# Kernel tuning notes

Hardware: AMD Instinct MI355X
Metric: run time of the kernel (lower is better)

The kernel has to match this reference:

```python
import jax, jax.numpy as jnp
import numpy as np

B, T = 64, 2048
QD, KD, VD, AD = 512, 512, 512, 256


def setup_inputs() -> dict:
    key = jax.random.key(0)
    ks = jax.random.split(key, 9)
    s = lambda d: 1.0 / np.sqrt(d)
    return {
        "query": jax.random.normal(ks[0], (B, QD), jnp.float32),
        "key": jax.random.normal(ks[1], (B, T, KD), jnp.float32),
        "value": jax.random.normal(ks[2], (B, T, VD), jnp.float32),
        "Wq": jax.random.uniform(ks[3], (QD, AD), jnp.float32, -s(QD), s(QD)),
        "bq": jax.random.uniform(ks[4], (AD,), jnp.float32, -s(QD), s(QD)),
        "Wk": jax.random.uniform(ks[5], (KD, AD), jnp.float32, -s(KD), s(KD)),
        "bk": jax.random.uniform(ks[6], (AD,), jnp.float32, -s(KD), s(KD)),
        "Wo": jax.random.uniform(ks[7], (AD, 1), jnp.float32, -s(AD), s(AD)),
        "bo": jax.random.uniform(ks[8], (1,), jnp.float32, -s(AD), s(AD)),
    }


def reference(query, key, value, Wq, bq, Wk, bk, Wo, bo):
    # q_proj: [B, 1, AD]; k_proj: [B, T, AD]
    q_proj = (query @ Wq + bq)[:, None, :]
    k_proj = jnp.einsum("btk,ka->bta", key, Wk) + bk
    # score: [B, T, 1]
    score = jnp.tanh(q_proj + k_proj) @ Wo + bo
    attn = jax.nn.softmax(score, axis=1)  # softmax over keys (dim 1)
    # context: [B, VD] = sum_t attn[b,t] * value[b,t,:]
    context = jnp.einsum("bt,btv->bv", attn[..., 0], value)
    return context, attn[..., 0]
```

## Files before the change

kernel.cpp:

```cpp
#include <hip/hip_runtime.h>

#define NB 64
#define NT 2048
#define NQD 512
#define NKD 512
#define NVD 512
#define NAD 256

typedef __attribute__((ext_vector_type(8))) short s16x8;
typedef __attribute__((ext_vector_type(4))) float fx4;
typedef __attribute__((ext_vector_type(4))) unsigned int u32x4;

__device__ __forceinline__ short f2bf(float x) {
  union { float f; unsigned u; } v; v.f = x;
  return (short)((v.u + 0x7fffu + ((v.u >> 16) & 1u)) >> 16);
}

__device__ __forceinline__ unsigned cvt_pk_bf16(float lo, float hi) {
  unsigned r;
  asm("v_cvt_pk_bf16_f32 %0, %1, %2" : "=v"(r) : "v"(lo), "v"(hi));
  return r;
}

__device__ __forceinline__ float fast_tanh(float x) {
  float e = __expf(x + x);
  return 1.0f - 2.0f * __builtin_amdgcn_rcpf(e + 1.0f);
}

__device__ __forceinline__ void cvt_write32(short* lds, int lbase, int swz, const fx4* q) {
  u32x4 w0, w1;
  w0[0] = cvt_pk_bf16(q[0][0], q[0][1]); w0[1] = cvt_pk_bf16(q[0][2], q[0][3]);
  w0[2] = cvt_pk_bf16(q[1][0], q[1][1]); w0[3] = cvt_pk_bf16(q[1][2], q[1][3]);
  w1[0] = cvt_pk_bf16(q[2][0], q[2][1]); w1[1] = cvt_pk_bf16(q[2][2], q[2][3]);
  w1[2] = cvt_pk_bf16(q[3][0], q[3][1]); w1[3] = cvt_pk_bf16(q[3][2], q[3][3]);
  *(u32x4*)((char*)lds + ((lbase) ^ swz)) = w0;
  *(u32x4*)((char*)lds + ((lbase + 16) ^ swz)) = w1;
}

__global__ void prep_kernel(const float* __restrict__ query, const float* __restrict__ Wq,
                            const float* __restrict__ bq, const float* __restrict__ bk,
                            const float* __restrict__ Wk,
                            float* __restrict__ qpk, short* __restrict__ Bpk) {
  __shared__ float q[NQD];
  const int tid = threadIdx.x;
  if (blockIdx.x < NB) {
    const int b = blockIdx.x;
    for (int k = tid; k < NQD; k += 256) q[k] = query[b * NQD + k];
    __syncthreads();
    float acc = bq[tid] + bk[tid];
#pragma unroll 8
    for (int k = 0; k < NQD; ++k) acc += q[k] * Wq[k * NAD + tid];
    qpk[b * NAD + tid] = acc;
  } else {
    const int ks = blockIdx.x - NB;
#pragma unroll
    for (int rep = 0; rep < 4; ++rep) {
      const int o = rep * 256 + tid;
      const int wnt = o >> 6;
      const int l = o & 63;
      const int g = l >> 4, h = l & 15;
      const int n = wnt * 16 + h;
      const int k0 = ks * 32 + g * 8;
      s16x8 v;
#pragma unroll
      for (int j = 0; j < 8; ++j) v[j] = f2bf(Wk[(size_t)(k0 + j) * NAD + n]);
      *(s16x8*)(Bpk + (size_t)(ks * 1024 + o) * 8) = v;
    }
  }
}

__global__ void __launch_bounds__(256, 3)
score_kernel(const float* __restrict__ key, const short* __restrict__ Bpk,
             const float* __restrict__ qpk, const float* __restrict__ Wo,
             float* __restrict__ score) {
  __shared__ short As[2][64 * 128];
  __shared__ float sred[4][64];
  const int tid = threadIdx.x;
  const int w = tid >> 6, l = tid & 63;
  const int g = l >> 4, h = l & 15;
  const int m0 = blockIdx.x * 64;
  const int b = m0 >> 11;

  const short* bbase = Bpk + (size_t)(w * 4 * 64 + l) * 8;

  s16x8 bcur[4];
#pragma unroll
  for (int nt = 0; nt < 4; ++nt) bcur[nt] = *(const s16x8*)(bbase + nt * 512);

  const int r = tid >> 3, kseg = tid & 7;
  const float* asrc0 = key + (size_t)(m0 + r) * NKD + kseg * 16;
  const float* asrc1 = asrc0 + (size_t)32 * NKD;
  const int lbase0 = r * 256 + kseg * 32;
  const int lbase1 = lbase0 + 32 * 256;
  const int swz = (r & 7) << 4;

  {
    fx4 st[8];
#pragma unroll
    for (int i = 0; i < 4; ++i) st[i] = *(const fx4*)(asrc0 + i * 4);
#pragma unroll
    for (int i = 0; i < 4; ++i) st[4 + i] = *(const fx4*)(asrc1 + i * 4);
    cvt_write32(&As[0][0], lbase0, swz, &st[0]);
    cvt_write32(&As[0][0], lbase1, swz, &st[4]);
  }
  __syncthreads();

  fx4 acc[4][4];
#pragma unroll
  for (int i = 0; i < 4; ++i)
#pragma unroll
    for (int j = 0; j < 4; ++j) acc[i][j] = fx4{0.f, 0.f, 0.f, 0.f};

  const int rsw = (h & 7) << 4;

  int buf = 0;
  for (int c = 0; c < 4; ++c) {
    const bool notLast = (c < 3);
    fx4 st[8];
    if (notLast) {
      const float* gp0 = asrc0 + (c + 1) * 128;
      const float* gp1 = asrc1 + (c + 1) * 128;
#pragma unroll
      for (int i = 0; i < 4; ++i) st[i] = *(const fx4*)(gp0 + i * 4);
#pragma unroll
      for (int i = 0; i < 4; ++i) st[4 + i] = *(const fx4*)(gp1 + i * 4);
    }
#pragma unroll
    for (int kl = 0; kl < 4; ++kl) {
      const int ks = c * 4 + kl;
      s16x8 bnxt[4];
      if (ks < 15) {
#pragma unroll
        for (int nt = 0; nt < 4; ++nt)
          bnxt[nt] = *(const s16x8*)(bbase + (size_t)(ks + 1) * 8192 + nt * 512);
      }
      s16x8 af[4];
#pragma unroll
      for (int mt = 0; mt < 4; ++mt)
        af[mt] = *(const s16x8*)((const char*)&As[buf][0] +
                                 (((mt * 16 + h) * 256 + kl * 64 + g * 16) ^ rsw));
#pragma unroll
      for (int mt = 0; mt < 4; ++mt)
#pragma unroll
        for (int nt = 0; nt < 4; ++nt)
          acc[mt][nt] = __builtin_amdgcn_mfma_f32_16x16x32_bf16(af[mt], bcur[nt], acc[mt][nt], 0, 0, 0);
      if (ks < 15) {
#pragma unroll
        for (int nt = 0; nt < 4; ++nt) bcur[nt] = bnxt[nt];
      }
    }
    if (notLast) {
      cvt_write32(&As[buf ^ 1][0], lbase0, swz, &st[0]);
      cvt_write32(&As[buf ^ 1][0], lbase1, swz, &st[4]);
    }
    __syncthreads();
    buf ^= 1;
  }

  float qv[4], wv[4];
#pragma unroll
  for (int nt = 0; nt < 4; ++nt) {
    const int n = w * 64 + nt * 16 + h;
    qv[nt] = qpk[b * NAD + n];
    wv[nt] = Wo[n];
  }
#pragma unroll
  for (int mt = 0; mt < 4; ++mt) {
#pragma unroll
    for (int rr = 0; rr < 4; ++rr) {
      float s = fast_tanh(acc[mt][0][rr] + qv[0]) * wv[0]
              + fast_tanh(acc[mt][1][rr] + qv[1]) * wv[1]
              + fast_tanh(acc[mt][2][rr] + qv[2]) * wv[2]
              + fast_tanh(acc[mt][3][rr] + qv[3]) * wv[3];
#pragma unroll
      for (int off = 1; off < 16; off <<= 1) s += __shfl_xor(s, off, 64);
      if (h == 0) sred[w][mt * 16 + g * 4 + rr] = s;
    }
  }
  __syncthreads();
  if (tid < 64)
    score[m0 + tid] = sred[0][tid] + sred[1][tid] + sred[2][tid] + sred[3][tid];
}

__global__ void softmax_kernel(const float* __restrict__ score, float* __restrict__ attn) {
  __shared__ float redm[4];
  __shared__ float reds[4];
  const int b = blockIdx.x, tid = threadIdx.x;
  const float* s = score + (size_t)b * NT;
  float v[8];
  float m = -3.0e38f;
#pragma unroll
  for (int j = 0; j < 8; ++j) { v[j] = s[tid + j * 256]; m = fmaxf(m, v[j]); }
#pragma unroll
  for (int off = 1; off < 64; off <<= 1) m = fmaxf(m, __shfl_xor(m, off, 64));
  if ((tid & 63) == 0) redm[tid >> 6] = m;
  __syncthreads();
  m = fmaxf(fmaxf(redm[0], redm[1]), fmaxf(redm[2], redm[3]));
  float sum = 0.f;
#pragma unroll
  for (int j = 0; j < 8; ++j) { v[j] = __expf(v[j] - m); sum += v[j]; }
#pragma unroll
  for (int off = 1; off < 64; off <<= 1) sum += __shfl_xor(sum, off, 64);
  if ((tid & 63) == 0) reds[tid >> 6] = sum;
  __syncthreads();
  sum = reds[0] + reds[1] + reds[2] + reds[3];
  const float inv = 1.0f / sum;
#pragma unroll
  for (int j = 0; j < 8; ++j) attn[(size_t)b * NT + tid + j * 256] = v[j] * inv;
}

__global__ void ctx_partial_kernel(const float* __restrict__ attn, const float* __restrict__ value,
                                   float* __restrict__ partial) {
  __shared__ float a[64];
  __shared__ fx4 red[128];
  const int blk = blockIdx.x;
  const int b = blk >> 5, tc = blk & 31;
  const int tid = threadIdx.x;
  if (tid < 64) a[tid] = attn[(size_t)b * NT + tc * 64 + tid];
  __syncthreads();
  const int half = tid >> 7;
  const int vi = (tid & 127) * 4;
  const float* vp = value + ((size_t)b * NT + tc * 64 + half) * NVD + vi;
  fx4 s = fx4{0.f, 0.f, 0.f, 0.f};
#pragma unroll 8
  for (int t = 0; t < 64; t += 2) {
    fx4 x = *(const fx4*)(vp + (size_t)t * NVD);
    const float wt = a[t + half];
    s += x * wt;
  }
  if (half) red[tid & 127] = s;
  __syncthreads();
  if (!half) {
    s += red[tid];
    *(fx4*)(partial + (size_t)blk * NVD + vi) = s;
  }
}

__global__ void ctx_reduce_kernel(const float* __restrict__ partial, float* __restrict__ ctx) {
  const int i = blockIdx.x * 256 + threadIdx.x;
  const int b = i >> 9, v = i & (NVD - 1);
  float s = 0.f;
#pragma unroll
  for (int tc = 0; tc < 32; ++tc) s += partial[(size_t)(b * 32 + tc) * NVD + v];
  ctx[i] = s;
}

extern "C" void kernel_launch(void* const* d_in, const int* in_sizes, int n_in,
                              void* d_out, int out_size, void* d_ws, size_t ws_size,
                              hipStream_t stream) {
  const float* query = (const float*)d_in[0];
  const float* key   = (const float*)d_in[1];
  const float* value = (const float*)d_in[2];
  const float* Wq    = (const float*)d_in[3];
  const float* bq    = (const float*)d_in[4];
  const float* Wk    = (const float*)d_in[5];
  const float* bk    = (const float*)d_in[6];
  const float* Wo    = (const float*)d_in[7];

  float* out  = (float*)d_out;
  float* ctx  = out;
  float* attn = out + NB * NVD;

  char* ws = (char*)d_ws;
  float* qpk     = (float*)(ws);
  short* Bpk     = (short*)(ws + 64 * 1024);
  float* score   = (float*)(ws + (64 + 256) * 1024);
  float* partial = (float*)(ws + (64 + 256 + 512) * 1024);

  prep_kernel<<<NB + 16, 256, 0, stream>>>(query, Wq, bq, bk, Wk, qpk, Bpk);
  score_kernel<<<(NB * NT) / 64, 256, 0, stream>>>(key, Bpk, qpk, Wo, score);
  softmax_kernel<<<NB, 256, 0, stream>>>(score, attn);
  ctx_partial_kernel<<<NB * 32, 256, 0, stream>>>(attn, value, partial);
  ctx_reduce_kernel<<<(NB * NVD) / 256, 256, 0, stream>>>(partial, ctx);
}
```

Before: 170.7 us.

## Fuse score, chunked softmax and context into one kernel with split-softmax combine

Each block now handles a 128-row chunk of one batch: it computes scores via MFMA for two 64-row tiles, does a local softmax (max and sum), writes unnormalized probabilities, and accumulates a partial context from value. A small combine kernel rescales the partial contexts and attn by the per-chunk max and sum statistics, as in flash-style split softmax. This removes the score round-trip and two launches. The grid shrinks from 2048 to 1024 blocks, and attn is written and then read back and rescaled.

```diff
diff --git a/kernel.cpp b/kernel.cpp
--- a/kernel.cpp
+++ b/kernel.cpp
@@ -6,6 +6,8 @@
 #define NKD 512
 #define NVD 512
 #define NAD 256
+#define NCH 16
+#define CHT 128
 
 typedef __attribute__((ext_vector_type(8))) short s16x8;
 typedef __attribute__((ext_vector_type(4))) float fx4;
@@ -70,179 +72,198 @@
 }
 
 __global__ void __launch_bounds__(256, 3)
-score_kernel(const float* __restrict__ key, const short* __restrict__ Bpk,
+fused_kernel(const float* __restrict__ key, const short* __restrict__ Bpk,
              const float* __restrict__ qpk, const float* __restrict__ Wo,
-             float* __restrict__ score) {
+             const float* __restrict__ value,
+             float* __restrict__ attn, float* __restrict__ stats,
+             float* __restrict__ partial) {
   __shared__ short As[2][64 * 128];
   __shared__ float sred[4][64];
+  __shared__ float pp[CHT];
+  __shared__ float red2[4];
+  __shared__ fx4 ctxred[128];
   const int tid = threadIdx.x;
   const int w = tid >> 6, l = tid & 63;
   const int g = l >> 4, h = l & 15;
-  const int m0 = blockIdx.x * 64;
-  const int b = m0 >> 11;
-
-  const short* bbase = Bpk + (size_t)(w * 4 * 64 + l) * 8;
-
-  s16x8 bcur[4];
-#pragma unroll
-  for (int nt = 0; nt < 4; ++nt) bcur[nt] = *(const s16x8*)(bbase + nt * 512);
-
+  const int b = blockIdx.x >> 4, tc = blockIdx.x & (NCH - 1);
+  const int trow0 = tc * CHT;
+
+  const short* bbase = Bpk + (size_t)(w * 256 + l) * 8;
   const int r = tid >> 3, kseg = tid & 7;
-  const float* asrc0 = key + (size_t)(m0 + r) * NKD + kseg * 16;
-  const float* asrc1 = asrc0 + (size_t)32 * NKD;
   const int lbase0 = r * 256 + kseg * 32;
   const int lbase1 = lbase0 + 32 * 256;
   const int swz = (r & 7) << 4;
-
+  const int rsw = (h & 7) << 4;
+
+#pragma unroll 1
+  for (int stile = 0; stile < 2; ++stile) {
+    const int m0 = b * NT + trow0 + stile * 64;
+    const float* asrc0 = key + (size_t)(m0 + r) * NKD + kseg * 16;
+    const float* asrc1 = asrc0 + (size_t)32 * NKD;
+
+    s16x8 bcur[4];
+#pragma unroll
+    for (int nt = 0; nt < 4; ++nt) bcur[nt] = *(const s16x8*)(bbase + nt * 512);
+
+    {
+      fx4 st[8];
+#pragma unroll
+      for (int i = 0; i < 4; ++i) st[i] = *(const fx4*)(asrc0 + i * 4);
+#pragma unroll
+      for (int i = 0; i < 4; ++i) st[4 + i] = *(const fx4*)(asrc1 + i * 4);
+      cvt_write32(&As[0][0], lbase0, swz, &st[0]);
+      cvt_write32(&As[0][0], lbase1, swz, &st[4]);
+    }
+    __syncthreads();
+
+    fx4 acc[4][4];
+#pragma unroll
+    for (int i = 0; i < 4; ++i)
+#pragma unroll
+      for (int j = 0; j < 4; ++j) acc[i][j] = fx4{0.f, 0.f, 0.f, 0.f};
+
+    int buf = 0;
+    for (int c = 0; c < 4; ++c) {
+      const bool notLast = (c < 3);
+      fx4 st[8];
+      if (notLast) {
+        const float* gp0 = asrc0 + (c + 1) * 128;
+        const float* gp1 = asrc1 + (c + 1) * 128;
+#pragma unroll
+        for (int i = 0; i < 4; ++i) st[i] = *(const fx4*)(gp0 + i * 4);
+#pragma unroll
+        for (int i = 0; i < 4; ++i) st[4 + i] = *(const fx4*)(gp1 + i * 4);
+      }
+#pragma unroll
+      for (int kl = 0; kl < 4; ++kl) {
+        const int ks = c * 4 + kl;
+        s16x8 bnxt[4];
+        if (ks < 15) {
+#pragma unroll
+          for (int nt = 0; nt < 4; ++nt)
+            bnxt[nt] = *(const s16x8*)(bbase + (size_t)(ks + 1) * 8192 + nt * 512);
+        }
+        s16x8 af[4];
+#pragma unroll
+        for (int mt = 0; mt < 4; ++mt)
+          af[mt] = *(const s16x8*)((const char*)&As[buf][0] +
+                                   (((mt * 16 + h) * 256 + kl * 64 + g * 16) ^ rsw));
+#pragma unroll
+        for (int mt = 0; mt < 4; ++mt)
+#pragma unroll
+          for (int nt = 0; nt < 4; ++nt)
+            acc[mt][nt] = __builtin_amdgcn_mfma_f32_16x16x32_bf16(af[mt], bcur[nt], acc[mt][nt], 0, 0, 0);
+        if (ks < 15) {
+#pragma unroll
+          for (int nt = 0; nt < 4; ++nt) bcur[nt] = bnxt[nt];
+        }
+      }
+      if (notLast) {
+        cvt_write32(&As[buf ^ 1][0], lbase0, swz, &st[0]);
+        cvt_write32(&As[buf ^ 1][0], lbase1, swz, &st[4]);
+      }
+      __syncthreads();
+      buf ^= 1;
+    }
+
+    float qv[4], wv[4];
+#pragma unroll
+    for (int nt = 0; nt < 4; ++nt) {
+      const int n = w * 64 + nt * 16 + h;
+      qv[nt] = qpk[b * NAD + n];
+      wv[nt] = Wo[n];
+    }
+#pragma unroll
+    for (int mt = 0; mt < 4; ++mt) {
+#pragma unroll
+      for (int rr = 0; rr < 4; ++rr) {
+        float s = fast_tanh(acc[mt][0][rr] + qv[0]) * wv[0]
+                + fast_tanh(acc[mt][1][rr] + qv[1]) * wv[1]
+                + fast_tanh(acc[mt][2][rr] + qv[2]) * wv[2]
+                + fast_tanh(acc[mt][3][rr] + qv[3]) * wv[3];
+#pragma unroll
+        for (int off = 1; off < 16; off <<= 1) s += __shfl_xor(s, off, 64);
+        if (h == 0) sred[w][mt * 16 + g * 4 + rr] = s;
+      }
+    }
+    __syncthreads();
+    if (tid < 64)
+      pp[stile * 64 + tid] = sred[0][tid] + sred[1][tid] + sred[2][tid] + sred[3][tid];
+    __syncthreads();
+  }
+
+  float m_loc, z_loc;
   {
-    fx4 st[8];
-#pragma unroll
-    for (int i = 0; i < 4; ++i) st[i] = *(const fx4*)(asrc0 + i * 4);
-#pragma unroll
-    for (int i = 0; i < 4; ++i) st[4 + i] = *(const fx4*)(asrc1 + i * 4);
-    cvt_write32(&As[0][0], lbase0, swz, &st[0]);
-    cvt_write32(&As[0][0], lbase1, swz, &st[4]);
-  }
+    const float v = (tid < CHT) ? pp[tid] : -3.0e38f;
+    float mm = v;
+#pragma unroll
+    for (int off = 1; off < 64; off <<= 1) mm = fmaxf(mm, __shfl_xor(mm, off, 64));
+    if (l == 0) red2[w] = mm;
+    __syncthreads();
+    m_loc = fmaxf(fmaxf(red2[0], red2[1]), fmaxf(red2[2], red2[3]));
+    const float p = (tid < CHT) ? __expf(v - m_loc) : 0.f;
+    float ss = p;
+#pragma unroll
+    for (int off = 1; off < 64; off <<= 1) ss += __shfl_xor(ss, off, 64);
+    __syncthreads();
+    if (l == 0) red2[w] = ss;
+    __syncthreads();
+    z_loc = red2[0] + red2[1] + red2[2] + red2[3];
+    if (tid < CHT) {
+      pp[tid] = p;
+      attn[(size_t)b * NT + trow0 + tid] = p;
+    }
+    if (tid == 0) {
+      stats[(b * NCH + tc) * 2] = m_loc;
+      stats[(b * NCH + tc) * 2 + 1] = z_loc;
+    }
+    __syncthreads();
+  }
+
+  {
+    const int half = tid >> 7;
+    const int vi = (tid & 127) * 4;
+    const float* vp = value + ((size_t)(b * NT + trow0 + half)) * NVD + vi;
+    fx4 s4 = fx4{0.f, 0.f, 0.f, 0.f};
+#pragma unroll 8
+    for (int t = 0; t < CHT; t += 2) {
+      fx4 x = *(const fx4*)(vp + (size_t)t * NVD);
+      s4 += x * pp[t + half];
+    }
+    if (half) ctxred[tid & 127] = s4;
+    __syncthreads();
+    if (!half) {
+      s4 += ctxred[tid];
+      *(fx4*)(partial + ((size_t)(b * NCH + tc)) * NVD + vi) = s4;
+    }
+  }
+}
+
+__global__ void combine_kernel(const float* __restrict__ stats, const float* __restrict__ partial,
+                               float* __restrict__ ctx, float* __restrict__ attn) {
+  __shared__ float scl[NCH];
+  const int b = blockIdx.x, tid = threadIdx.x;
+  float m = -3.0e38f;
+#pragma unroll
+  for (int c = 0; c < NCH; ++c) m = fmaxf(m, stats[(b * NCH + c) * 2]);
+  float Z = 0.f;
+#pragma unroll
+  for (int c = 0; c < NCH; ++c)
+    Z += stats[(b * NCH + c) * 2 + 1] * __expf(stats[(b * NCH + c) * 2] - m);
+  const float inv = 1.0f / Z;
+  if (tid < NCH) scl[tid] = __expf(stats[(b * NCH + tid) * 2] - m);
   __syncthreads();
-
-  fx4 acc[4][4];
-#pragma unroll
-  for (int i = 0; i < 4; ++i)
-#pragma unroll
-    for (int j = 0; j < 4; ++j) acc[i][j] = fx4{0.f, 0.f, 0.f, 0.f};
-
-  const int rsw = (h & 7) << 4;
-
-  int buf = 0;
-  for (int c = 0; c < 4; ++c) {
-    const bool notLast = (c < 3);
-    fx4 st[8];
-    if (notLast) {
-      const float* gp0 = asrc0 + (c + 1) * 128;
-      const float* gp1 = asrc1 + (c + 1) * 128;
-#pragma unroll
-      for (int i = 0; i < 4; ++i) st[i] = *(const fx4*)(gp0 + i * 4);
-#pragma unroll
-      for (int i = 0; i < 4; ++i) st[4 + i] = *(const fx4*)(gp1 + i * 4);
-    }
-#pragma unroll
-    for (int kl = 0; kl < 4; ++kl) {
-      const int ks = c * 4 + kl;
-      s16x8 bnxt[4];
-      if (ks < 15) {
-#pragma unroll
-        for (int nt = 0; nt < 4; ++nt)
-          bnxt[nt] = *(const s16x8*)(bbase + (size_t)(ks + 1) * 8192 + nt * 512);
-      }
-      s16x8 af[4];
-#pragma unroll
-      for (int mt = 0; mt < 4; ++mt)
-        af[mt] = *(const s16x8*)((const char*)&As[buf][0] +
-                                 (((mt * 16 + h) * 256 + kl * 64 + g * 16) ^ rsw));
-#pragma unroll
-      for (int mt = 0; mt < 4; ++mt)
-#pragma unroll
-        for (int nt = 0; nt < 4; ++nt)
-          acc[mt][nt] = __builtin_amdgcn_mfma_f32_16x16x32_bf16(af[mt], bcur[nt], acc[mt][nt], 0, 0, 0);
-      if (ks < 15) {
-#pragma unroll
-        for (int nt = 0; nt < 4; ++nt) bcur[nt] = bnxt[nt];
-      }
-    }
-    if (notLast) {
-      cvt_write32(&As[buf ^ 1][0], lbase0, swz, &st[0]);
-      cvt_write32(&As[buf ^ 1][0], lbase1, swz, &st[4]);
-    }
-    __syncthreads();
-    buf ^= 1;
-  }
-
-  float qv[4], wv[4];
-#pragma unroll
-  for (int nt = 0; nt < 4; ++nt) {
-    const int n = w * 64 + nt * 16 + h;
-    qv[nt] = qpk[b * NAD + n];
-    wv[nt] = Wo[n];
-  }
-#pragma unroll
-  for (int mt = 0; mt < 4; ++mt) {
-#pragma unroll
-    for (int rr = 0; rr < 4; ++rr) {
-      float s = fast_tanh(acc[mt][0][rr] + qv[0]) * wv[0]
-              + fast_tanh(acc[mt][1][rr] + qv[1]) * wv[1]
-              + fast_tanh(acc[mt][2][rr] + qv[2]) * wv[2]
-              + fast_tanh(acc[mt][3][rr] + qv[3]) * wv[3];
-#pragma unroll
-      for (int off = 1; off < 16; off <<= 1) s += __shfl_xor(s, off, 64);
-      if (h == 0) sred[w][mt * 16 + g * 4 + rr] = s;
-    }
-  }
-  __syncthreads();
-  if (tid < 64)
-    score[m0 + tid] = sred[0][tid] + sred[1][tid] + sred[2][tid] + sred[3][tid];
-}
-
-__global__ void softmax_kernel(const float* __restrict__ score, float* __restrict__ attn) {
-  __shared__ float redm[4];
-  __shared__ float reds[4];
-  const int b = blockIdx.x, tid = threadIdx.x;
-  const float* s = score + (size_t)b * NT;
-  float v[8];
-  float m = -3.0e38f;
-#pragma unroll
-  for (int j = 0; j < 8; ++j) { v[j] = s[tid + j * 256]; m = fmaxf(m, v[j]); }
-#pragma unroll
-  for (int off = 1; off < 64; off <<= 1) m = fmaxf(m, __shfl_xor(m, off, 64));
-  if ((tid & 63) == 0) redm[tid >> 6] = m;
-  __syncthreads();
-  m = fmaxf(fmaxf(redm[0], redm[1]), fmaxf(redm[2], redm[3]));
-  float sum = 0.f;
-#pragma unroll
-  for (int j = 0; j < 8; ++j) { v[j] = __expf(v[j] - m); sum += v[j]; }
-#pragma unroll
-  for (int off = 1; off < 64; off <<= 1) sum += __shfl_xor(sum, off, 64);
-  if ((tid & 63) == 0) reds[tid >> 6] = sum;
-  __syncthreads();
-  sum = reds[0] + reds[1] + reds[2] + reds[3];
-  const float inv = 1.0f / sum;
-#pragma unroll
-  for (int j = 0; j < 8; ++j) attn[(size_t)b * NT + tid + j * 256] = v[j] * inv;
-}
-
-__global__ void ctx_partial_kernel(const float* __restrict__ attn, const float* __restrict__ value,
-                                   float* __restrict__ partial) {
-  __shared__ float a[64];
-  __shared__ fx4 red[128];
-  const int blk = blockIdx.x;
-  const int b = blk >> 5, tc = blk & 31;
-  const int tid = threadIdx.x;
-  if (tid < 64) a[tid] = attn[(size_t)b * NT + tc * 64 + tid];
-  __syncthreads();
-  const int half = tid >> 7;
-  const int vi = (tid & 127) * 4;
-  const float* vp = value + ((size_t)b * NT + tc * 64 + half) * NVD + vi;
-  fx4 s = fx4{0.f, 0.f, 0.f, 0.f};
-#pragma unroll 8
-  for (int t = 0; t < 64; t += 2) {
-    fx4 x = *(const fx4*)(vp + (size_t)t * NVD);
-    const float wt = a[t + half];
-    s += x * wt;
-  }
-  if (half) red[tid & 127] = s;
-  __syncthreads();
-  if (!half) {
-    s += red[tid];
-    *(fx4*)(partial + (size_t)blk * NVD + vi) = s;
-  }
-}
-
-__global__ void ctx_reduce_kernel(const float* __restrict__ partial, float* __restrict__ ctx) {
-  const int i = blockIdx.x * 256 + threadIdx.x;
-  const int b = i >> 9, v = i & (NVD - 1);
-  float s = 0.f;
-#pragma unroll
-  for (int tc = 0; tc < 32; ++tc) s += partial[(size_t)(b * 32 + tc) * NVD + v];
-  ctx[i] = s;
+#pragma unroll
+  for (int i = tid; i < NVD; i += 256) {
+    float s = 0.f;
+#pragma unroll
+    for (int c = 0; c < NCH; ++c) s += partial[(size_t)(b * NCH + c) * NVD + i] * scl[c];
+    ctx[b * NVD + i] = s * inv;
+  }
+#pragma unroll
+  for (int j = tid; j < NT; j += 256) {
+    attn[(size_t)b * NT + j] *= scl[j >> 7] * inv;
+  }
 }
 
 extern "C" void kernel_launch(void* const* d_in, const int* in_sizes, int n_in,
@@ -264,12 +285,10 @@
   char* ws = (char*)d_ws;
   float* qpk     = (float*)(ws);
   short* Bpk     = (short*)(ws + 64 * 1024);
-  float* score   = (float*)(ws + (64 + 256) * 1024);
-  float* partial = (float*)(ws + (64 + 256 + 512) * 1024);
+  float* stats   = (float*)(ws + 320 * 1024);
+  float* partial = (float*)(ws + 384 * 1024);
 
   prep_kernel<<<NB + 16, 256, 0, stream>>>(query, Wq, bq, bk, Wk, qpk, Bpk);
-  score_kernel<<<(NB * NT) / 64, 256, 0, stream>>>(key, Bpk, qpk, Wo, score);
-  softmax_kernel<<<NB, 256, 0, stream>>>(score, attn);
-  ctx_partial_kernel<<<NB * 32, 256, 0, stream>>>(attn, value, partial);
-  ctx_reduce_kernel<<<(NB * NVD) / 256, 256, 0, stream>>>(partial, ctx);
-}
+  fused_kernel<<<NB * NCH, 256, 0, stream>>>(key, Bpk, qpk, Wo, value, attn, stats, partial);
+  combine_kernel<<<NB, 256, 0, stream>>>(stats, partial, ctx, attn);
+}
```

Result: slower. 258.0 us (+51.1%).
